# Kernel tuning notes

Hardware: AMD Instinct MI355X
Metric: run time of the kernel (lower is better)

The kernel has to match this reference:

```python
import jax, jax.numpy as jnp
import numpy as np

H, HD, C = 16, 64, 64            # num_heads, head_dim, mini_batch_size
BASE_LR = 1.0
EPS = 1e-6                        # ttt LN eps (ln_fwd / ln_fused_l2_bwd)


def _l2norm(x):
    return x / jnp.maximum(jnp.linalg.norm(x, axis=-1, keepdims=True), 1e-12)


def _ln_fwd(x, g, b):
    mu = x.mean(-1, keepdims=True)
    var = x.var(-1, keepdims=True)
    return g * ((x - mu) * jax.lax.rsqrt(var + EPS)) + b


def _ln_l2_bwd(x, tgt, g, b):
    # gradient of ||LN(x)*g+b - tgt||^2 / 2 wrt x
    D = x.shape[-1]
    mu = x.mean(-1, keepdims=True)
    var = x.var(-1, keepdims=True)
    std = jnp.sqrt(var + EPS)
    xh = (x - mu) / std
    gout = (g * xh + b) - tgt
    gxh = gout * g
    return (D * gxh - gxh.sum(-1, keepdims=True) - xh * (gxh * xh).sum(-1, keepdims=True)) / (D * std)


def setup_inputs() -> dict:
    key = jax.random.key(0)
    ks = jax.random.split(key, 12)
    B, L, D = 4, 8192, 1024
    std = 0.02
    return {
        'hidden_states': jax.random.normal(ks[0], (B, L, D), jnp.float32),
        'wq_w': jax.random.normal(ks[1], (D, D), jnp.float32) * std,
        'wq_b': jnp.zeros((D,), jnp.float32),
        'wk_w': jax.random.normal(ks[2], (D, D), jnp.float32) * std,
        'wk_b': jnp.zeros((D,), jnp.float32),
        'wv_w': jax.random.normal(ks[3], (D, D), jnp.float32) * std,
        'wv_b': jnp.zeros((D,), jnp.float32),
        'wo_w': jax.random.normal(ks[4], (D, D), jnp.float32) * std,
        'wo_b': jnp.zeros((D,), jnp.float32),
        'ttt_norm_weight': jnp.ones((H, HD), jnp.float32),
        'ttt_norm_bias': jnp.zeros((H, HD), jnp.float32),
        'ttt_lr_weight': jax.random.normal(ks[5], (H, 1, D), jnp.float32) * std,
        'ttt_lr_bias': jnp.zeros((H, 1), jnp.float32),
        'W1': jax.random.normal(ks[6], (H, HD, HD), jnp.float32) * std,
        'b1': jnp.zeros((H, 1, HD), jnp.float32),
        'post_norm_w': jnp.ones((D,), jnp.float32),
        'post_norm_b': jnp.zeros((D,), jnp.float32),
    }


def _forward(hidden_states, wq_w, wq_b, wk_w, wk_b, wv_w, wv_b, wo_w, wo_b,
             ttt_norm_weight, ttt_norm_bias, ttt_lr_weight, ttt_lr_bias,
             W1, b1, post_norm_w, post_norm_b):
    B, L, D = hidden_states.shape
    NC = L // C
    XQ = (hidden_states @ wq_w.T + wq_b).reshape(B, L, H, HD)
    XK = (hidden_states @ wk_w.T + wk_b).reshape(B, L, H, HD)
    XV = (hidden_states @ wv_w.T + wv_b).reshape(B, L, H, HD)
    XQ = _l2norm(XQ)
    XK = _l2norm(XK)
    # ln_reconstruction_target (uses sample std, ddof=1, eps=1e-5 on std)
    d = XV - XK
    mu = d.mean(-1, keepdims=True)
    sd = d.std(-1, keepdims=True, ddof=1)
    XV = ttt_norm_weight[None, None] * ((d - mu) / (sd + 1e-5)) + ttt_norm_bias[None, None] + XK
    # reshape to mini-batches: [B,H,NC,C,HD]
    Xmb = hidden_states.reshape(B, NC, C, D)
    to_mb = lambda t: t.transpose(0, 2, 1, 3).reshape(B, H, NC, C, HD)
    XQ, XK, XV = to_mb(XQ), to_mb(XK), to_mb(XV)
    # eta: sigmoid lr gate per token, row-broadcast over mini-batch
    ttt_lr = jax.nn.sigmoid(jnp.einsum('bnkc,hdc->bhnkd', Xmb, ttt_lr_weight)
                            + ttt_lr_bias.reshape(1, H, 1, 1, 1))     # [B,H,NC,C,1]
    eta = jnp.swapaxes(ttt_lr, -1, -2) * (BASE_LR / HD / C)           # [B,H,NC,1,C]
    mask = jnp.tril(jnp.ones((C, C), hidden_states.dtype))
    g = ttt_norm_weight[None, :, None, :]
    bta = ttt_norm_bias[None, :, None, :]
    W0 = jnp.broadcast_to(W1[None], (B, H, HD, HD))
    b0 = jnp.broadcast_to(b1[None], (B, H, 1, HD))

    def step(carry, xs):
        W, bvec = carry
        xq, xk, xv, eta_row = xs                      # eta_row: [B,H,1,C]
        Z1 = xk @ W + bvec                            # [B,H,C,HD]
        grad = _ln_l2_bwd(Z1, xv - xk, g, bta)        # [B,H,C,HD]
        Attn = mask * jnp.einsum('bhid,bhjd->bhij', xq, xk)   # [B,H,C,C]
        eta_full = jnp.broadcast_to(eta_row, Attn.shape)      # [B,H,C,C]
        b1_bar = bvec - (mask * eta_full) @ grad              # [B,H,C,HD]
        Z1_bar = xq @ W - (eta_full * Attn) @ grad + b1_bar
        last_eta = eta_full[..., -1, :, None]                 # [B,H,C,1]
        W_new = W - jnp.einsum('bhcd,bhce->bhde', last_eta * xk, grad)
        b_new = bvec - (last_eta * grad).sum(-2, keepdims=True)
        out = xq + _ln_fwd(Z1_bar, g, bta)
        return (W_new, b_new), out

    xs = (jnp.moveaxis(XQ, 2, 0), jnp.moveaxis(XK, 2, 0),
          jnp.moveaxis(XV, 2, 0), jnp.moveaxis(eta, 2, 0))
    _, outs = jax.lax.scan(step, (W0, b0), xs)        # outs: [NC,B,H,C,HD]
    y = jnp.moveaxis(outs, 0, 2).reshape(B, H, L, HD).transpose(0, 2, 1, 3).reshape(B, L, D)
    # post LayerNorm (eps=1e-6) + output projection
    mu2 = y.mean(-1, keepdims=True)
    var2 = y.var(-1, keepdims=True)
    y = post_norm_w * ((y - mu2) * jax.lax.rsqrt(var2 + 1e-6)) + post_norm_b
    return y @ wo_w.T + wo_b


def reference(hidden_states, wq_w, wq_b, wk_w, wk_b, wv_w, wv_b, wo_w, wo_b,
              ttt_norm_weight, ttt_norm_bias, ttt_lr_weight, ttt_lr_bias,
              W1, b1, post_norm_w, post_norm_b):
    return _forward(hidden_states, wq_w, wq_b, wk_w, wk_b, wv_w, wv_b, wo_w, wo_b,
                    ttt_norm_weight, ttt_norm_bias, ttt_lr_weight, ttt_lr_bias,
                    W1, b1, post_norm_w, post_norm_b)
```

## Files before the change

### kernel.cpp

```cpp
#include <hip/hip_runtime.h>


typedef __attribute__((ext_vector_type(8))) short short8;
typedef __attribute__((ext_vector_type(4))) float f32x4;
typedef __attribute__((ext_vector_type(4))) unsigned short us4;

__device__ __forceinline__ float bf2f(unsigned short s) {
  union { unsigned int u; float f; } c;
  c.u = ((unsigned int)s) << 16;
  return c.f;
}
__device__ __forceinline__ unsigned short f2bf(float f) {
  union { float f; unsigned int u; } c;
  c.f = f;
  unsigned int u = c.u;
  return (unsigned short)((u + 0x7FFFu + ((u >> 16) & 1u)) >> 16);
}

__device__ __forceinline__ void gload_lds16(const void* g, void* l) {
  __builtin_amdgcn_global_load_lds(
      (const __attribute__((address_space(1))) unsigned int*)g,
      (__attribute__((address_space(3))) unsigned int*)l, 16, 0, 0);
}

__device__ __forceinline__ float dpp16_sum(float x) {
  int v = __float_as_int(x);
  x += __int_as_float(__builtin_amdgcn_update_dpp(v, v, 0xB1, 0xF, 0xF, true));
  v = __float_as_int(x);
  x += __int_as_float(__builtin_amdgcn_update_dpp(v, v, 0x4E, 0xF, 0xF, true));
  v = __float_as_int(x);
  x += __int_as_float(__builtin_amdgcn_update_dpp(v, v, 0x141, 0xF, 0xF, true));
  v = __float_as_int(x);
  x += __int_as_float(__builtin_amdgcn_update_dpp(v, v, 0x140, 0xF, 0xF, true));
  return x;
}

__device__ __forceinline__ void barrier_fast() {
  __builtin_amdgcn_sched_barrier(0);
  asm volatile("s_waitcnt lgkmcnt(0)" ::: "memory");
  __builtin_amdgcn_s_barrier();
  asm volatile("" ::: "memory");
  __builtin_amdgcn_sched_barrier(0);
}
__device__ __forceinline__ void bar_nowait() {
  __builtin_amdgcn_sched_barrier(0);
  asm volatile("" ::: "memory");
  __builtin_amdgcn_s_barrier();
  asm volatile("" ::: "memory");
  __builtin_amdgcn_sched_barrier(0);
}

__global__ __launch_bounds__(256) void cvt_f32_bf16(
    const float* __restrict__ in, unsigned short* __restrict__ out, long n) {
  long i = ((long)blockIdx.x * 256 + threadIdx.x) * 4;
  if (i + 3 < n) {
    float4 v = *(const float4*)&in[i];
    us4 o = { f2bf(v.x), f2bf(v.y), f2bf(v.z), f2bf(v.w) };
    *(us4*)&out[i] = o;
  }
}

__global__ __launch_bounds__(256) void build_wcat(
    const float* __restrict__ wq, const float* __restrict__ wk,
    const float* __restrict__ wv, const float* __restrict__ lrw,
    const float* __restrict__ wqb, const float* __restrict__ wkb,
    const float* __restrict__ wvb, const float* __restrict__ lrb,
    unsigned short* __restrict__ Wcat, float* __restrict__ biasc) {
  int i = blockIdx.x * 256 + threadIdx.x;
  int row = i >> 10, col = i & 1023;
  int h = row >> 8, o = row & 255;
  float v;
  if (o < 64)        v = wq[(h * 64 + o) * 1024 + col];
  else if (o < 128)  v = wk[(h * 64 + o - 64) * 1024 + col];
  else if (o < 192)  v = wv[(h * 64 + o - 128) * 1024 + col];
  else if (o == 192) v = lrw[h * 1024 + col];
  else               v = 0.f;
  Wcat[i] = f2bf(v);
  if (i < 4096) {
    int hh = i >> 8, oo = i & 255;
    float bv;
    if (oo < 64)        bv = wqb[hh * 64 + oo];
    else if (oo < 128)  bv = wkb[hh * 64 + oo - 64];
    else if (oo < 192)  bv = wvb[hh * 64 + oo - 128];
    else if (oo == 192) bv = lrb[hh];
    else                bv = 0.f;
    biasc[i] = bv;
  }
}

__global__ __launch_bounds__(512, 1) void gemm256_qkv(
    const unsigned short* __restrict__ A, const unsigned short* __restrict__ B,
    const float* __restrict__ bias, const float* __restrict__ tnw,
    const float* __restrict__ tnb, unsigned short* __restrict__ XQn,
    unsigned short* __restrict__ XKn, unsigned short* __restrict__ TGT,
    float* __restrict__ eta, long M, long K) {
  __shared__ __align__(16) unsigned short g_lds[65536];
  char* ldsc = (char*)g_lds;
  const int tid = threadIdx.x, lane = tid & 63, wid = tid >> 6;
  const int wm = wid >> 2, wn = wid & 3;
  const int l15 = lane & 15, lg = lane >> 4;
  const int NTILN = 16;

  unsigned nwg = gridDim.x, bid = blockIdx.x;
  unsigned cpx = nwg >> 3;
  unsigned swz = (bid & 7) * cpx + (bid >> 3);
  unsigned nidx = swz % (unsigned)NTILN, midx = swz / (unsigned)NTILN;
  const long m0 = (long)midx * 256, n0 = (long)nidx * 256;
  const long ldab = K * 2;

  const int srow = wid * 16 + (lane >> 2);
  const int scol = ((lane & 3) * 16) ^ (((lane >> 3) & 3) << 4);
  const int sdst = wid * 1024;
  const char* Ab = (const char*)A;
  const char* Bb = (const char*)B;

  const int acol = (lg * 16) ^ (((l15 >> 1) & 3) << 4);
  const int aro = (wm * 128 + l15) * 64 + acol;
  const int bro = 65536 + (wn * 64 + l15) * 64 + acol;

#define STG_A(tt, h, bb)                                                      \
  gload_lds16(Ab + (size_t)(m0 + (h) * 128 + srow) * ldab + (size_t)(tt) * 64 \
                  + scol,                                                     \
              ldsc + (bb) * 16384 + (h) * 8192 + sdst)
#define STG_B(tt, h, bb)                                                      \
  gload_lds16(Bb + (size_t)(n0 + (h) * 128 + srow) * ldab + (size_t)(tt) * 64 \
                  + scol,                                                     \
              ldsc + 65536 + (bb) * 16384 + (h) * 8192 + sdst)

  f32x4 acc[8][4];
#pragma unroll
  for (int m = 0; m < 8; ++m)
#pragma unroll
    for (int n = 0; n < 4; ++n) acc[m][n] = (f32x4){0.f, 0.f, 0.f, 0.f};

  const int NT = (int)(K >> 5);

#pragma unroll
  for (int tt = 0; tt < 3; ++tt) {
    STG_A(tt, 0, tt); STG_A(tt, 1, tt);
    STG_B(tt, 0, tt); STG_B(tt, 1, tt);
  }
  asm volatile("s_waitcnt vmcnt(8)" ::: "memory");
  bar_nowait();

#pragma unroll 1
  for (int t = 0; t < NT; ++t) {
    const int buf = t & 3, sb = (t + 3) & 3;
    const bool doStage = (t + 3 < NT);
    const char* ab = ldsc + buf * 16384 + aro;
    const char* bb = ldsc + buf * 16384 + bro;

    short8 av[4], bv[4];
#pragma unroll
    for (int i = 0; i < 4; ++i) av[i] = *(const short8*)(ab + i * 1024);
#pragma unroll
    for (int nf = 0; nf < 4; ++nf) bv[nf] = *(const short8*)(bb + nf * 1024);
    if (doStage) { STG_A(t + 3, 0, sb); STG_A(t + 3, 1, sb); }
    bar_nowait();
    __builtin_amdgcn_s_setprio(1);
#pragma unroll
    for (int i = 0; i < 4; ++i)
#pragma unroll
      for (int nf = 0; nf < 4; ++nf)
        acc[i][nf] = __builtin_amdgcn_mfma_f32_16x16x32_bf16(av[i], bv[nf],
                                                             acc[i][nf], 0, 0, 0);
    __builtin_amdgcn_s_setprio(0);
    bar_nowait();

#pragma unroll
    for (int i = 0; i < 4; ++i) av[i] = *(const short8*)(ab + 4096 + i * 1024);
    if (doStage) { STG_B(t + 3, 0, sb); STG_B(t + 3, 1, sb); }
    bar_nowait();
    __builtin_amdgcn_s_setprio(1);
#pragma unroll
    for (int i = 0; i < 4; ++i)
#pragma unroll
      for (int nf = 0; nf < 4; ++nf)
        acc[4 + i][nf] = __builtin_amdgcn_mfma_f32_16x16x32_bf16(
            av[i], bv[nf], acc[4 + i][nf], 0, 0, 0);
    __builtin_amdgcn_s_setprio(0);
    asm volatile("s_waitcnt vmcnt(8)" ::: "memory");
    bar_nowait();
  }
#undef STG_A
#undef STG_B

  const int h = (int)nidx;
  float bcol[4], twv[4], tbv[4];
#pragma unroll
  for (int nf = 0; nf < 4; ++nf) {
    bcol[nf] = bias[n0 + wn * 64 + nf * 16 + l15];
    twv[nf] = tnw[h * 64 + nf * 16 + l15];
    tbv[nf] = tnb[h * 64 + nf * 16 + l15];
  }
  __syncthreads();
  unsigned short* kn_s = g_lds;

  if (wn == 0) {
#pragma unroll
    for (int mf = 0; mf < 8; ++mf)
#pragma unroll
      for (int j = 0; j < 4; ++j) {
        float v[4], s2 = 0.f;
#pragma unroll
        for (int nf = 0; nf < 4; ++nf) {
          v[nf] = acc[mf][nf][j] + bcol[nf];
          s2 += v[nf] * v[nf];
        }
        s2 = dpp16_sum(s2);
        float rn = 1.f / fmaxf(sqrtf(s2), 1e-12f);
        size_t tt = (size_t)(m0 + wm * 128 + mf * 16 + lg * 4 + j);
#pragma unroll
        for (int nf = 0; nf < 4; ++nf)
          XQn[tt * 1024 + h * 64 + nf * 16 + l15] = f2bf(v[nf] * rn);
      }
  } else if (wn == 1) {
#pragma unroll
    for (int mf = 0; mf < 8; ++mf)
#pragma unroll
      for (int j = 0; j < 4; ++j) {
        float v[4], s2 = 0.f;
#pragma unroll
        for (int nf = 0; nf < 4; ++nf) {
          v[nf] = acc[mf][nf][j] + bcol[nf];
          s2 += v[nf] * v[nf];
        }
        s2 = dpp16_sum(s2);
        float rn = 1.f / fmaxf(sqrtf(s2), 1e-12f);
        size_t tt = (size_t)(m0 + wm * 128 + mf * 16 + lg * 4 + j);
        int lr_ = wm * 128 + mf * 16 + lg * 4 + j;
#pragma unroll
        for (int nf = 0; nf < 4; ++nf) {
          unsigned short kb = f2bf(v[nf] * rn);
          XKn[tt * 1024 + h * 64 + nf * 16 + l15] = kb;
          kn_s[lr_ * 72 + nf * 16 + l15] = kb;
        }
      }
  }
  __syncthreads();
  if (wn == 2) {
#pragma unroll
    for (int mf = 0; mf < 8; ++mf)
#pragma unroll
      for (int j = 0; j < 4; ++j) {
        int lr_ = wm * 128 + mf * 16 + lg * 4 + j;
        float dv[4], s1 = 0.f, s2 = 0.f;
#pragma unroll
        for (int nf = 0; nf < 4; ++nf) {
          float kn = bf2f(kn_s[lr_ * 72 + nf * 16 + l15]);
          dv[nf] = acc[mf][nf][j] + bcol[nf] - kn;
          s1 += dv[nf];
          s2 += dv[nf] * dv[nf];
        }
        s1 = dpp16_sum(s1);
        s2 = dpp16_sum(s2);
        float mu = s1 * 0.015625f;
        float var1 = fmaxf(s2 - 64.f * mu * mu, 0.f) * (1.f / 63.f);
        float rs = 1.f / (sqrtf(var1) + 1e-5f);
        size_t tt = (size_t)(m0 + wm * 128 + mf * 16 + lg * 4 + j);
#pragma unroll
        for (int nf = 0; nf < 4; ++nf)
          TGT[tt * 1024 + h * 64 + nf * 16 + l15] =
              f2bf(twv[nf] * ((dv[nf] - mu) * rs) + tbv[nf]);
      }
  } else if (wn == 3 && l15 == 0) {
#pragma unroll
    for (int mf = 0; mf < 8; ++mf)
#pragma unroll
      for (int j = 0; j < 4; ++j) {
        size_t tt = (size_t)(m0 + wm * 128 + mf * 16 + lg * 4 + j);
        float lgt = acc[mf][0][j] + bcol[0];
        float sig = 1.f / (1.f + expf(-lgt));
        eta[((tt >> 13) * 16 + h) * 8192 + (tt & 8191)] = sig * (1.f / 4096.f);
      }
  }
}

template <int WRITE_BF16>
__global__ __launch_bounds__(512, 1) void gemm256(
    const unsigned short* __restrict__ A, const unsigned short* __restrict__ B,
    const float* __restrict__ bias, void* __restrict__ Cout,
    long M, long N, long K, int NTILN, long ldc) {
  __shared__ __align__(16) unsigned short g_lds[65536];
  char* ldsc = (char*)g_lds;
  const int tid = threadIdx.x, lane = tid & 63, wid = tid >> 6;
  const int wm = wid >> 2, wn = wid & 3;
  const int l15 = lane & 15, lg = lane >> 4;

  unsigned nwg = gridDim.x, bid = blockIdx.x;
  unsigned cpx = nwg >> 3;
  unsigned swz = (bid & 7) * cpx + (bid >> 3);
  unsigned nidx = swz % (unsigned)NTILN, midx = swz / (unsigned)NTILN;
  const long m0 = (long)midx * 256, n0 = (long)nidx * 256;
  const long ldab = K * 2;

  const int srow = wid * 16 + (lane >> 2);
  const int scol = ((lane & 3) * 16) ^ (((lane >> 3) & 3) << 4);
  const int sdst = wid * 1024;
  const char* Ab = (const char*)A;
  const char* Bb = (const char*)B;

  const int acol = (lg * 16) ^ (((l15 >> 1) & 3) << 4);
  const int aro = (wm * 128 + l15) * 64 + acol;
  const int bro = 65536 + (wn * 64 + l15) * 64 + acol;

#define STG_A(tt, h, bb)                                                      \
  gload_lds16(Ab + (size_t)(m0 + (h) * 128 + srow) * ldab + (size_t)(tt) * 64 \
                  + scol,                                                     \
              ldsc + (bb) * 16384 + (h) * 8192 + sdst)
#define STG_B(tt, h, bb)                                                      \
  gload_lds16(Bb + (size_t)(n0 + (h) * 128 + srow) * ldab + (size_t)(tt) * 64 \
                  + scol,                                                     \
              ldsc + 65536 + (bb) * 16384 + (h) * 8192 + sdst)

  f32x4 acc[8][4];
#pragma unroll
  for (int m = 0; m < 8; ++m)
#pragma unroll
    for (int n = 0; n < 4; ++n) acc[m][n] = (f32x4){0.f, 0.f, 0.f, 0.f};

  const int NT = (int)(K >> 5);

#pragma unroll
  for (int tt = 0; tt < 3; ++tt) {
    STG_A(tt, 0, tt); STG_A(tt, 1, tt);
    STG_B(tt, 0, tt); STG_B(tt, 1, tt);
  }
  asm volatile("s_waitcnt vmcnt(8)" ::: "memory");
  bar_nowait();

#pragma unroll 1
  for (int t = 0; t < NT; ++t) {
    const int buf = t & 3, sb = (t + 3) & 3;
    const bool doStage = (t + 3 < NT);
    const char* ab = ldsc + buf * 16384 + aro;
    const char* bb = ldsc + buf * 16384 + bro;

    short8 av[4], bv[4];
#pragma unroll
    for (int i = 0; i < 4; ++i) av[i] = *(const short8*)(ab + i * 1024);
#pragma unroll
    for (int nf = 0; nf < 4; ++nf) bv[nf] = *(const short8*)(bb + nf * 1024);
    if (doStage) { STG_A(t + 3, 0, sb); STG_A(t + 3, 1, sb); }
    bar_nowait();
    __builtin_amdgcn_s_setprio(1);
#pragma unroll
    for (int i = 0; i < 4; ++i)
#pragma unroll
      for (int nf = 0; nf < 4; ++nf)
        acc[i][nf] = __builtin_amdgcn_mfma_f32_16x16x32_bf16(av[i], bv[nf],
                                                             acc[i][nf], 0, 0, 0);
    __builtin_amdgcn_s_setprio(0);
    bar_nowait();

#pragma unroll
    for (int i = 0; i < 4; ++i) av[i] = *(const short8*)(ab + 4096 + i * 1024);
    if (doStage) { STG_B(t + 3, 0, sb); STG_B(t + 3, 1, sb); }
    bar_nowait();
    __builtin_amdgcn_s_setprio(1);
#pragma unroll
    for (int i = 0; i < 4; ++i)
#pragma unroll
      for (int nf = 0; nf < 4; ++nf)
        acc[4 + i][nf] = __builtin_amdgcn_mfma_f32_16x16x32_bf16(
            av[i], bv[nf], acc[4 + i][nf], 0, 0, 0);
    __builtin_amdgcn_s_setprio(0);
    asm volatile("s_waitcnt vmcnt(8)" ::: "memory");
    bar_nowait();
  }
#undef STG_A
#undef STG_B

#pragma unroll
  for (int mf = 0; mf < 8; ++mf) {
    long r0 = m0 + wm * 128 + mf * 16 + lg * 4;
#pragma unroll
    for (int nf = 0; nf < 4; ++nf) {
      long c = n0 + wn * 64 + nf * 16 + l15;
      float bvv = bias ? bias[c] : 0.f;
#pragma unroll
      for (int j = 0; j < 4; ++j) {
        float v = acc[mf][nf][j] + bvv;
        if (WRITE_BF16)
          ((unsigned short*)Cout)[(r0 + j) * ldc + c] = f2bf(v);
        else
          ((float*)Cout)[(r0 + j) * ldc + c] = v;
      }
    }
  }
}

__global__ __launch_bounds__(512, 1) void ttt_scan(
    const unsigned short* __restrict__ XQ, const unsigned short* __restrict__ XK,
    const unsigned short* __restrict__ TG, const float* __restrict__ eta_buf,
    const float* __restrict__ W1, const float* __restrict__ b1,
    const float* __restrict__ tnw, const float* __restrict__ tnb,
    float* __restrict__ y) {
  const int bh = blockIdx.x;
  const int b = bh >> 4, h = bh & 15;
  const int tid = threadIdx.x;
  const int lane = tid & 63, wid = tid >> 6;
  const bool isA = wid < 4;
  const int q = wid & 3;
  const int l15 = lane & 15, lg = lane >> 4;

  __shared__ __align__(16) unsigned short xq_s[2][64 * 72];
  __shared__ __align__(16) unsigned short tg_s[2][64 * 72];
  __shared__ __align__(16) unsigned short xk_s[2][64 * 72];
  __shared__ __align__(16) unsigned short gc_s[64 * 72];
  __shared__ __align__(16) unsigned short gradT[64 * 72];
  __shared__ __align__(16) unsigned short xkTe[64 * 72];
  __shared__ __align__(16) unsigned short WT_b[2][64 * 72];
  __shared__ float eta_s[2][64];
  __shared__ float bpart[4][64];

  const size_t tokb = (size_t)b * 8192;
  const int col0 = h * 64;
  const int rr_ = q * 16 + (lane >> 3);
  const int c8_ = (lane & 7) * 8;

  short8 pA0[2], pA1[2], pB0[2];
  float peta = 0.f;
  float bstv[4], gwv[4], gbv[4];
  f32x4 Wreg[4];

  if (isA) {
#pragma unroll
    for (int n = 0; n < 4; ++n) {
      int e = n * 16 + l15;
      bstv[n] = b1[h * 64 + e];
      gwv[n] = tnw[h * 64 + e];
      gbv[n] = tnb[h * 64 + e];
    }
#pragma unroll
    for (int j = 0; j < 2; ++j) {
      size_t g = (tokb + rr_ + j * 8) * 1024 + col0 + c8_;
      pA0[j] = *(const short8*)&XQ[g];
      pA1[j] = *(const short8*)&TG[g];
    }
#pragma unroll
    for (int j = 0; j < 2; ++j) {
      int rr = rr_ + j * 8;
      *(short8*)&xq_s[0][rr * 72 + c8_] = pA0[j];
      *(short8*)&tg_s[0][rr * 72 + c8_] = pA1[j];
    }
#pragma unroll
    for (int j = 0; j < 2; ++j) {
      size_t g = (tokb + 64 + rr_ + j * 8) * 1024 + col0 + c8_;
      pA0[j] = *(const short8*)&XQ[g];
      pA1[j] = *(const short8*)&TG[g];
    }
  } else {
#pragma unroll
    for (int j = 0; j < 2; ++j)
      pB0[j] = *(const short8*)&XK[(tokb + rr_ + j * 8) * 1024 + col0 + c8_];
#pragma unroll
    for (int j = 0; j < 2; ++j)
      *(short8*)&xk_s[0][(rr_ + j * 8) * 72 + c8_] = pB0[j];
#pragma unroll
    for (int j = 0; j < 2; ++j)
      pB0[j] = *(const short8*)&XK[(tokb + 64 + rr_ + j * 8) * 1024 + col0 + c8_];
#pragma unroll
    for (int n = 0; n < 4; ++n)
#pragma unroll
      for (int jj = 0; jj < 4; ++jj) {
        int d = q * 16 + lg * 4 + jj, e = n * 16 + l15;
        float w = W1[h * 4096 + d * 64 + e];
        Wreg[n][jj] = w;
        WT_b[0][e * 72 + d] = f2bf(w);
      }
    if (wid == 4) {
      eta_s[0][lane] = eta_buf[(size_t)bh * 8192 + lane];
      peta = eta_buf[(size_t)bh * 8192 + 64 + lane];
    }
  }
  __syncthreads();

  for (int nc = 0; nc < 128; ++nc) {
    const int p = nc & 1;
    const unsigned short* WTc = WT_b[p];
    unsigned short* WTn = WT_b[p ^ 1];

    if (isA) {
      if (nc) {
#pragma unroll
        for (int n = 0; n < 4; ++n) {
          int e = n * 16 + l15;
          bstv[n] -= bpart[0][e] + bpart[1][e] + bpart[2][e] + bpart[3][e];
        }
      }
      if (nc + 1 < 128) {
#pragma unroll
        for (int j = 0; j < 2; ++j) {
          int rr = rr_ + j * 8;
          *(short8*)&xq_s[p ^ 1][rr * 72 + c8_] = pA0[j];
          *(short8*)&tg_s[p ^ 1][rr * 72 + c8_] = pA1[j];
        }
      }
      if (nc + 2 < 128) {
#pragma unroll
        for (int j = 0; j < 2; ++j) {
          size_t g = (tokb + (nc + 2) * 64 + rr_ + j * 8) * 1024 + col0 + c8_;
          pA0[j] = *(const short8*)&XQ[g];
          pA1[j] = *(const short8*)&TG[g];
        }
      }
      f32x4 accZ[4];
#pragma unroll
      for (int n = 0; n < 4; ++n)
        accZ[n] = (f32x4){bstv[n], bstv[n], bstv[n], bstv[n]};
      __builtin_amdgcn_s_setprio(1);
#pragma unroll
      for (int kk = 0; kk < 2; ++kk) {
        const int ko = kk * 32 + lg * 8;
        short8 a_xk = *(const short8*)&xk_s[p][(q * 16 + l15) * 72 + ko];
#pragma unroll
        for (int n = 0; n < 4; ++n) {
          short8 b_w = *(const short8*)&WTc[(n * 16 + l15) * 72 + ko];
          accZ[n] = __builtin_amdgcn_mfma_f32_16x16x32_bf16(a_xk, b_w, accZ[n], 0, 0, 0);
        }
      }
      __builtin_amdgcn_s_setprio(0);
      float grv[4][4];
#pragma unroll
      for (int j = 0; j < 4; ++j) {
        const int r = q * 16 + lg * 4 + j;
        float z[4], s1 = 0.f, s2 = 0.f;
#pragma unroll
        for (int n = 0; n < 4; ++n) {
          z[n] = accZ[n][j];
          s1 += z[n];
          s2 += z[n] * z[n];
        }
        s1 = dpp16_sum(s1);
        s2 = dpp16_sum(s2);
        float mu = s1 * 0.015625f;
        float var = s2 * 0.015625f - mu * mu;
        float rstd = rsqrtf(var + 1e-6f);
        float xh[4], gx[4], s3 = 0.f, s4 = 0.f;
#pragma unroll
        for (int n = 0; n < 4; ++n) {
          xh[n] = (z[n] - mu) * rstd;
          float tg = bf2f(tg_s[p][r * 72 + n * 16 + l15]);
          float go = gwv[n] * xh[n] + gbv[n] - tg;
          gx[n] = go * gwv[n];
          s3 += gx[n];
          s4 += gx[n] * xh[n];
        }
        s3 = dpp16_sum(s3);
        s4 = dpp16_sum(s4);
#pragma unroll
        for (int n = 0; n < 4; ++n)
          grv[n][j] = (64.f * gx[n] - s3 - xh[n] * s4) * rstd * 0.015625f;
      }
#pragma unroll
      for (int n = 0; n < 4; ++n) {
        us4 pk = {f2bf(grv[n][0]), f2bf(grv[n][1]), f2bf(grv[n][2]),
                  f2bf(grv[n][3])};
        *(us4*)&gradT[(n * 16 + l15) * 72 + q * 16 + lg * 4] = pk;
      }
    } else {
      if (nc + 1 < 128) {
#pragma unroll
        for (int j = 0; j < 2; ++j)
          *(short8*)&xk_s[p ^ 1][(rr_ + j * 8) * 72 + c8_] = pB0[j];
        if (wid == 4) eta_s[p ^ 1][lane] = peta;
      }
      if (nc + 2 < 128) {
#pragma unroll
        for (int j = 0; j < 2; ++j)
          pB0[j] = *(const short8*)
              &XK[(tokb + (nc + 2) * 64 + rr_ + j * 8) * 1024 + col0 + c8_];
        if (wid == 4) peta = eta_buf[(size_t)bh * 8192 + (nc + 2) * 64 + lane];
      }
#pragma unroll
      for (int it = 0; it < 4; ++it) {
        int c0 = q * 16 + it * 4;
        us4 pk;
#pragma unroll
        for (int u = 0; u < 4; ++u)
          pk[u] = f2bf(-eta_s[p][c0 + u] * bf2f(xk_s[p][(c0 + u) * 72 + lane]));
        *(us4*)&xkTe[lane * 72 + c0] = pk;
      }
      f32x4 accA[4];
#pragma unroll
      for (int n = 0; n < 4; ++n) accA[n] = (f32x4){0.f, 0.f, 0.f, 0.f};
      __builtin_amdgcn_s_setprio(1);
#pragma unroll
      for (int kk = 0; kk < 2; ++kk) {
        const int ko = kk * 32 + lg * 8;
        short8 a_xq = *(const short8*)&xq_s[p][(q * 16 + l15) * 72 + ko];
#pragma unroll
        for (int n = 0; n < 4; ++n) {
          short8 b_k = *(const short8*)&xk_s[p][(n * 16 + l15) * 72 + ko];
          accA[n] = __builtin_amdgcn_mfma_f32_16x16x32_bf16(a_xq, b_k, accA[n], 0, 0, 0);
        }
      }
      __builtin_amdgcn_s_setprio(0);
#pragma unroll
      for (int j = 0; j < 4; ++j) {
        const int r = q * 16 + lg * 4 + j;
#pragma unroll
        for (int n = 0; n < 4; ++n) {
          int cj = n * 16 + l15;
          float v = (cj <= r) ? (-eta_s[p][cj] * (1.f + accA[n][j])) : 0.f;
          gc_s[r * 72 + cj] = f2bf(v);
        }
      }
    }
    barrier_fast();

    if (isA) {
      f32x4 accZb[4];
#pragma unroll
      for (int n = 0; n < 4; ++n)
        accZb[n] = (f32x4){bstv[n], bstv[n], bstv[n], bstv[n]};
      __builtin_amdgcn_s_setprio(1);
#pragma unroll
      for (int kk = 0; kk < 2; ++kk) {
        const int ko = kk * 32 + lg * 8;
        short8 a_xq = *(const short8*)&xq_s[p][(q * 16 + l15) * 72 + ko];
        short8 a_gc = *(const short8*)&gc_s[(q * 16 + l15) * 72 + ko];
#pragma unroll
        for (int n = 0; n < 4; ++n) {
          short8 b_w = *(const short8*)&WTc[(n * 16 + l15) * 72 + ko];
          short8 b_g = *(const short8*)&gradT[(n * 16 + l15) * 72 + ko];
          accZb[n] = __builtin_amdgcn_mfma_f32_16x16x32_bf16(a_xq, b_w, accZb[n], 0, 0, 0);
          accZb[n] = __builtin_amdgcn_mfma_f32_16x16x32_bf16(a_gc, b_g, accZb[n], 0, 0, 0);
        }
      }
      __builtin_amdgcn_s_setprio(0);
#pragma unroll
      for (int j = 0; j < 4; ++j) {
        const int r = q * 16 + lg * 4 + j;
        float z[4], s1 = 0.f, s2 = 0.f;
#pragma unroll
        for (int n = 0; n < 4; ++n) {
          z[n] = accZb[n][j];
          s1 += z[n];
          s2 += z[n] * z[n];
        }
        s1 = dpp16_sum(s1);
        s2 = dpp16_sum(s2);
        float mu = s1 * 0.015625f;
        float var = s2 * 0.015625f - mu * mu;
        float rstd = rsqrtf(var + 1e-6f);
        size_t gbase = (tokb + nc * 64 + r) * 1024 + col0;
#pragma unroll
        for (int n = 0; n < 4; ++n) {
          int e = n * 16 + l15;
          float ov = bf2f(xq_s[p][r * 72 + e]) + gwv[n] * ((z[n] - mu) * rstd) + gbv[n];
          y[gbase + e] = ov;
        }
      }
    } else {
      short8 a_ke[2], b_g[2][4];
#pragma unroll
      for (int kk = 0; kk < 2; ++kk) {
        const int ko = kk * 32 + lg * 8;
        a_ke[kk] = *(const short8*)&xkTe[(q * 16 + l15) * 72 + ko];
#pragma unroll
        for (int n = 0; n < 4; ++n)
          b_g[kk][n] = *(const short8*)&gradT[(n * 16 + l15) * 72 + ko];
      }
      f32x4 accW[4];
#pragma unroll
      for (int n = 0; n < 4; ++n) accW[n] = Wreg[n];
      __builtin_amdgcn_s_setprio(1);
#pragma unroll
      for (int kk = 0; kk < 2; ++kk)
#pragma unroll
        for (int n = 0; n < 4; ++n)
          accW[n] = __builtin_amdgcn_mfma_f32_16x16x32_bf16(a_ke[kk], b_g[kk][n],
                                                            accW[n], 0, 0, 0);
      __builtin_amdgcn_s_setprio(0);
#pragma unroll
      for (int n = 0; n < 4; ++n) {
        Wreg[n] = accW[n];
        us4 pk = {f2bf(accW[n][0]), f2bf(accW[n][1]), f2bf(accW[n][2]),
                  f2bf(accW[n][3])};
        *(us4*)&WTn[(n * 16 + l15) * 72 + q * 16 + lg * 4] = pk;
      }
      {
        float s = 0.f;
#pragma unroll
        for (int it = 0; it < 4; ++it) {
          us4 gv = *(const us4*)&gradT[lane * 72 + q * 16 + it * 4];
#pragma unroll
          for (int u = 0; u < 4; ++u)
            s += eta_s[p][q * 16 + it * 4 + u] * bf2f(gv[u]);
        }
        bpart[q][lane] = s;
      }
    }
    barrier_fast();
  }
}

__global__ __launch_bounds__(256) void postnorm(
    const float* __restrict__ yv, const float* __restrict__ pw,
    const float* __restrict__ pb, unsigned short* __restrict__ yn) {
  int t = blockIdx.x;
  int tid = threadIdx.x, lane = tid & 63, wid = tid >> 6;
  const float* row = yv + (size_t)t * 1024;
  float4 v = *(const float4*)&row[tid * 4];
  float s1 = v.x + v.y + v.z + v.w;
  float s2 = v.x * v.x + v.y * v.y + v.z * v.z + v.w * v.w;
#pragma unroll
  for (int o = 1; o < 64; o <<= 1) {
    s1 += __shfl_xor(s1, o);
    s2 += __shfl_xor(s2, o);
  }
  __shared__ float r1[4], r2[4];
  if (lane == 0) {
    r1[wid] = s1;
    r2[wid] = s2;
  }
  __syncthreads();
  s1 = r1[0] + r1[1] + r1[2] + r1[3];
  s2 = r2[0] + r2[1] + r2[2] + r2[3];
  float mu = s1 * (1.f / 1024.f);
  float var = s2 * (1.f / 1024.f) - mu * mu;
  float rstd = rsqrtf(var + 1e-6f);
  int c = tid * 4;
  us4 o4 = {f2bf(pw[c] * ((v.x - mu) * rstd) + pb[c]),
            f2bf(pw[c + 1] * ((v.y - mu) * rstd) + pb[c + 1]),
            f2bf(pw[c + 2] * ((v.z - mu) * rstd) + pb[c + 2]),
            f2bf(pw[c + 3] * ((v.w - mu) * rstd) + pb[c + 3])};
  *(us4*)&yn[(size_t)t * 1024 + c] = o4;
}

extern "C" void kernel_launch(void* const* d_in, const int* in_sizes, int n_in,
                              void* d_out, int out_size, void* d_ws,
                              size_t ws_size, hipStream_t stream) {
  const float* hs  = (const float*)d_in[0];
  const float* wqw = (const float*)d_in[1];
  const float* wqb = (const float*)d_in[2];
  const float* wkw = (const float*)d_in[3];
  const float* wkb = (const float*)d_in[4];
  const float* wvw = (const float*)d_in[5];
  const float* wvb = (const float*)d_in[6];
  const float* wow = (const float*)d_in[7];
  const float* wob = (const float*)d_in[8];
  const float* tnw = (const float*)d_in[9];
  const float* tnb = (const float*)d_in[10];
  const float* lrw = (const float*)d_in[11];
  const float* lrb = (const float*)d_in[12];
  const float* W1  = (const float*)d_in[13];
  const float* b1  = (const float*)d_in[14];
  const float* pnw = (const float*)d_in[15];
  const float* pnb = (const float*)d_in[16];

  const size_t OFF_XQ    = 0;
  const size_t OFF_XK    = 67108864;
  const size_t OFF_TGT   = 134217728;
  const size_t OFF_ETA   = 201326592;
  const size_t OFF_WOBF  = OFF_ETA + 2097152;
  const size_t OFF_HSBF  = OFF_WOBF + 2097152;
  const size_t OFF_WCAT  = OFF_HSBF + 67108864;
  const size_t OFF_BIASC = OFF_WCAT + 8388608;
  const size_t OFF_YV    = OFF_HSBF;
  const size_t NEEDED_A  = OFF_BIASC + 16384;
  const size_t NEEDED_B  = OFF_YV + 134217728;
  const size_t NEEDED    = NEEDED_A > NEEDED_B ? NEEDED_A : NEEDED_B;
  if (ws_size < NEEDED) return;

  char* ws = (char*)d_ws;
  unsigned short* XQn   = (unsigned short*)(ws + OFF_XQ);
  unsigned short* ynorm = (unsigned short*)(ws + OFF_XQ);
  unsigned short* XKn   = (unsigned short*)(ws + OFF_XK);
  unsigned short* TGT   = (unsigned short*)(ws + OFF_TGT);
  float* eta_buf        = (float*)(ws + OFF_ETA);
  unsigned short* wo_bf = (unsigned short*)(ws + OFF_WOBF);
  unsigned short* hs_bf = (unsigned short*)(ws + OFF_HSBF);
  unsigned short* Wcat  = (unsigned short*)(ws + OFF_WCAT);
  float* biasc          = (float*)(ws + OFF_BIASC);
  float* yv             = (float*)(ws + OFF_YV);

  cvt_f32_bf16<<<32768, 256, 0, stream>>>(hs, hs_bf, 33554432L);
  build_wcat<<<16384, 256, 0, stream>>>(wqw, wkw, wvw, lrw, wqb, wkb, wvb, lrb,
                                        Wcat, biasc);
  cvt_f32_bf16<<<1024, 256, 0, stream>>>(wow, wo_bf, 1048576L);
  gemm256_qkv<<<2048, 512, 0, stream>>>(hs_bf, Wcat, biasc, tnw, tnb,
                                        XQn, XKn, TGT, eta_buf, 32768L, 1024L);
  ttt_scan<<<64, 512, 0, stream>>>(XQn, XKn, TGT, eta_buf, W1, b1, tnw, tnb, yv);
  postnorm<<<32768, 256, 0, stream>>>(yv, pnw, pnb, ynorm);
  gemm256<0><<<512, 512, 0, stream>>>(ynorm, wo_bf, wob, d_out,
                                      32768L, 1024L, 1024L, 4, 1024L);
}
```

Baseline: 889.4 us.

## Stage projection epilogue through LDS for coalesced stores and swizzle xkTe

The QKV projection epilogue now writes normalized Q, K and the LN target into LDS tiles, then copies them to global memory as 16-byte row-contiguous chunks. This replaces scattered 2-byte stores, and idle waves handle the Q/K copy while the target is computed. Separately, the transposed eta*xk tile in the scan kernel gets an XOR swizzle on its 4-element groups to reduce LDS bank conflicts on the write and the MFMA operand read. The cost is an extra barrier, more LDS traffic, and a chance that the swizzle indexing is wrong.

```diff
diff --git a/kernel.cpp b/kernel.cpp
--- a/kernel.cpp
+++ b/kernel.cpp
@@ -194,7 +194,9 @@
     tbv[nf] = tnb[h * 64 + nf * 16 + l15];
   }
   __syncthreads();
-  unsigned short* kn_s = g_lds;
+  unsigned short* kn_t = g_lds;
+  unsigned short* qn_t = g_lds + 18432;
+  unsigned short* tg_t = g_lds + 36864;
 
   if (wn == 0) {
 #pragma unroll
@@ -209,10 +211,10 @@
         }
         s2 = dpp16_sum(s2);
         float rn = 1.f / fmaxf(sqrtf(s2), 1e-12f);
-        size_t tt = (size_t)(m0 + wm * 128 + mf * 16 + lg * 4 + j);
+        int lr_ = wm * 128 + mf * 16 + lg * 4 + j;
 #pragma unroll
         for (int nf = 0; nf < 4; ++nf)
-          XQn[tt * 1024 + h * 64 + nf * 16 + l15] = f2bf(v[nf] * rn);
+          qn_t[lr_ * 72 + nf * 16 + l15] = f2bf(v[nf] * rn);
       }
   } else if (wn == 1) {
 #pragma unroll
@@ -227,17 +229,24 @@
         }
         s2 = dpp16_sum(s2);
         float rn = 1.f / fmaxf(sqrtf(s2), 1e-12f);
+        int lr_ = wm * 128 + mf * 16 + lg * 4 + j;
+#pragma unroll
+        for (int nf = 0; nf < 4; ++nf)
+          kn_t[lr_ * 72 + nf * 16 + l15] = f2bf(v[nf] * rn);
+      }
+  } else if (wn == 3 && l15 == 0) {
+#pragma unroll
+    for (int mf = 0; mf < 8; ++mf)
+#pragma unroll
+      for (int j = 0; j < 4; ++j) {
         size_t tt = (size_t)(m0 + wm * 128 + mf * 16 + lg * 4 + j);
-        int lr_ = wm * 128 + mf * 16 + lg * 4 + j;
-#pragma unroll
-        for (int nf = 0; nf < 4; ++nf) {
-          unsigned short kb = f2bf(v[nf] * rn);
-          XKn[tt * 1024 + h * 64 + nf * 16 + l15] = kb;
-          kn_s[lr_ * 72 + nf * 16 + l15] = kb;
-        }
+        float lgt = acc[mf][0][j] + bcol[0];
+        float sig = 1.f / (1.f + expf(-lgt));
+        eta[((tt >> 13) * 16 + h) * 8192 + (tt & 8191)] = sig * (1.f / 4096.f);
       }
   }
   __syncthreads();
+
   if (wn == 2) {
 #pragma unroll
     for (int mf = 0; mf < 8; ++mf)
@@ -247,7 +256,7 @@
         float dv[4], s1 = 0.f, s2 = 0.f;
 #pragma unroll
         for (int nf = 0; nf < 4; ++nf) {
-          float kn = bf2f(kn_s[lr_ * 72 + nf * 16 + l15]);
+          float kn = bf2f(kn_t[lr_ * 72 + nf * 16 + l15]);
           dv[nf] = acc[mf][nf][j] + bcol[nf] - kn;
           s1 += dv[nf];
           s2 += dv[nf] * dv[nf];
@@ -257,22 +266,27 @@
         float mu = s1 * 0.015625f;
         float var1 = fmaxf(s2 - 64.f * mu * mu, 0.f) * (1.f / 63.f);
         float rs = 1.f / (sqrtf(var1) + 1e-5f);
-        size_t tt = (size_t)(m0 + wm * 128 + mf * 16 + lg * 4 + j);
 #pragma unroll
         for (int nf = 0; nf < 4; ++nf)
-          TGT[tt * 1024 + h * 64 + nf * 16 + l15] =
+          tg_t[lr_ * 72 + nf * 16 + l15] =
               f2bf(twv[nf] * ((dv[nf] - mu) * rs) + tbv[nf]);
       }
-  } else if (wn == 3 && l15 == 0) {
-#pragma unroll
-    for (int mf = 0; mf < 8; ++mf)
-#pragma unroll
-      for (int j = 0; j < 4; ++j) {
-        size_t tt = (size_t)(m0 + wm * 128 + mf * 16 + lg * 4 + j);
-        float lgt = acc[mf][0][j] + bcol[0];
-        float sig = 1.f / (1.f + expf(-lgt));
-        eta[((tt >> 13) * 16 + h) * 8192 + (tt & 8191)] = sig * (1.f / 4096.f);
-      }
+  } else {
+    int wlin = wid - (wid >= 3) - (wid >= 7);
+    const unsigned short* src = (wlin < 3) ? qn_t : kn_t;
+    unsigned short* dst = (wlin < 3) ? XQn : XKn;
+    int wl = wlin % 3;
+    for (int c = wl * 64 + lane; c < 2048; c += 192) {
+      int r = c >> 3, ch = c & 7;
+      short8 v = *(const short8*)&src[r * 72 + ch * 8];
+      *(short8*)&dst[(m0 + r) * 1024 + h * 64 + ch * 8] = v;
+    }
+  }
+  __syncthreads();
+  for (int c = tid; c < 2048; c += 512) {
+    int r = c >> 3, ch = c & 7;
+    short8 v = *(const short8*)&tg_t[r * 72 + ch * 8];
+    *(short8*)&TGT[(m0 + r) * 1024 + h * 64 + ch * 8] = v;
   }
 }
 
@@ -573,14 +587,17 @@
               &XK[(tokb + (nc + 2) * 64 + rr_ + j * 8) * 1024 + col0 + c8_];
         if (wid == 4) peta = eta_buf[(size_t)bh * 8192 + (nc + 2) * 64 + lane];
       }
-#pragma unroll
-      for (int it = 0; it < 4; ++it) {
-        int c0 = q * 16 + it * 4;
-        us4 pk;
-#pragma unroll
-        for (int u = 0; u < 4; ++u)
-          pk[u] = f2bf(-eta_s[p][c0 + u] * bf2f(xk_s[p][(c0 + u) * 72 + lane]));
-        *(us4*)&xkTe[lane * 72 + c0] = pk;
+      {
+        const int sxk = ((lane >> 3) & 3) << 1;
+#pragma unroll
+        for (int it = 0; it < 4; ++it) {
+          int c0 = q * 16 + it * 4;
+          us4 pk;
+#pragma unroll
+          for (int u = 0; u < 4; ++u)
+            pk[u] = f2bf(-eta_s[p][c0 + u] * bf2f(xk_s[p][(c0 + u) * 72 + lane]));
+          *(us4*)&xkTe[lane * 72 + (((q * 4 + it) ^ sxk) << 2)] = pk;
+        }
       }
       f32x4 accA[4];
 #pragma unroll
@@ -654,14 +671,15 @@
         }
       }
     } else {
+      const int scons = ((2 * q + (l15 >> 3)) & 3) << 1;
       short8 a_ke[2], b_g[2][4];
 #pragma unroll
       for (int kk = 0; kk < 2; ++kk) {
-        const int ko = kk * 32 + lg * 8;
-        a_ke[kk] = *(const short8*)&xkTe[(q * 16 + l15) * 72 + ko];
+        const int gb = (kk * 8 + lg * 2) ^ scons;
+        a_ke[kk] = *(const short8*)&xkTe[(q * 16 + l15) * 72 + (gb << 2)];
 #pragma unroll
         for (int n = 0; n < 4; ++n)
-          b_g[kk][n] = *(const short8*)&gradT[(n * 16 + l15) * 72 + ko];
+          b_g[kk][n] = *(const short8*)&gradT[(n * 16 + l15) * 72 + kk * 32 + lg * 8];
       }
       f32x4 accW[4];
 #pragma unroll
```

New measurement: 901.3 us. About the same (+1.3%).

## Switch GEMM mainloops to 3-stage interleaved A/B LDS pipeline with one barrier

Applied to the files above, without the earlier changes.

Both 256x256 GEMM kernels move from a 4-deep buffer ring with A and B in separate LDS regions to a 3-deep ring where each stage holds A and B together. Each iteration now issues all four stage loads up front, reads all eight A fragments at once, runs 32 MFMAs in one block and hits a single barrier instead of three. The LDS footprint shrinks from 128 KB to 96 KB. The trade-offs are a shallower prefetch distance, more live A registers, and a possible read-after-overwrite race, since stage t+2 is issued into a buffer without a fresh barrier.

```diff
diff --git a/kernel.cpp b/kernel.cpp
--- a/kernel.cpp
+++ b/kernel.cpp
@@ -88,13 +88,14 @@
   }
 }
 
+
 __global__ __launch_bounds__(512, 1) void gemm256_qkv(
     const unsigned short* __restrict__ A, const unsigned short* __restrict__ B,
     const float* __restrict__ bias, const float* __restrict__ tnw,
     const float* __restrict__ tnb, unsigned short* __restrict__ XQn,
     unsigned short* __restrict__ XKn, unsigned short* __restrict__ TGT,
     float* __restrict__ eta, long M, long K) {
-  __shared__ __align__(16) unsigned short g_lds[65536];
+  __shared__ __align__(16) unsigned short g_lds[49152];
   char* ldsc = (char*)g_lds;
   const int tid = threadIdx.x, lane = tid & 63, wid = tid >> 6;
   const int wm = wid >> 2, wn = wid & 3;
@@ -116,16 +117,16 @@
 
   const int acol = (lg * 16) ^ (((l15 >> 1) & 3) << 4);
   const int aro = (wm * 128 + l15) * 64 + acol;
-  const int bro = 65536 + (wn * 64 + l15) * 64 + acol;
+  const int bro = 16384 + (wn * 64 + l15) * 64 + acol;
 
 #define STG_A(tt, h, bb)                                                      \
   gload_lds16(Ab + (size_t)(m0 + (h) * 128 + srow) * ldab + (size_t)(tt) * 64 \
                   + scol,                                                     \
-              ldsc + (bb) * 16384 + (h) * 8192 + sdst)
+              ldsc + (bb) * 32768 + (h) * 8192 + sdst)
 #define STG_B(tt, h, bb)                                                      \
   gload_lds16(Bb + (size_t)(n0 + (h) * 128 + srow) * ldab + (size_t)(tt) * 64 \
                   + scol,                                                     \
-              ldsc + 65536 + (bb) * 16384 + (h) * 8192 + sdst)
+              ldsc + (bb) * 32768 + 16384 + (h) * 8192 + sdst)
 
   f32x4 acc[8][4];
 #pragma unroll
@@ -135,52 +136,37 @@
 
   const int NT = (int)(K >> 5);
 
-#pragma unroll
-  for (int tt = 0; tt < 3; ++tt) {
-    STG_A(tt, 0, tt); STG_A(tt, 1, tt);
-    STG_B(tt, 0, tt); STG_B(tt, 1, tt);
-  }
-  asm volatile("s_waitcnt vmcnt(8)" ::: "memory");
+  STG_A(0, 0, 0); STG_A(0, 1, 0); STG_B(0, 0, 0); STG_B(0, 1, 0);
+  STG_A(1, 0, 1); STG_A(1, 1, 1); STG_B(1, 0, 1); STG_B(1, 1, 1);
+  asm volatile("s_waitcnt vmcnt(4)" ::: "memory");
   bar_nowait();
 
+  int buf = 0, sb = 2;
 #pragma unroll 1
   for (int t = 0; t < NT; ++t) {
-    const int buf = t & 3, sb = (t + 3) & 3;
-    const bool doStage = (t + 3 < NT);
-    const char* ab = ldsc + buf * 16384 + aro;
-    const char* bb = ldsc + buf * 16384 + bro;
-
-    short8 av[4], bv[4];
-#pragma unroll
-    for (int i = 0; i < 4; ++i) av[i] = *(const short8*)(ab + i * 1024);
-#pragma unroll
-    for (int nf = 0; nf < 4; ++nf) bv[nf] = *(const short8*)(bb + nf * 1024);
-    if (doStage) { STG_A(t + 3, 0, sb); STG_A(t + 3, 1, sb); }
-    bar_nowait();
+    if (t + 2 < NT) {
+      STG_A(t + 2, 0, sb); STG_A(t + 2, 1, sb);
+      STG_B(t + 2, 0, sb); STG_B(t + 2, 1, sb);
+    }
+    const char* ab = ldsc + buf * 32768 + aro;
+    const char* bb2 = ldsc + buf * 32768 + bro;
+    short8 av[8], bv[4];
+#pragma unroll
+    for (int i = 0; i < 8; ++i) av[i] = *(const short8*)(ab + i * 1024);
+#pragma unroll
+    for (int nf = 0; nf < 4; ++nf) bv[nf] = *(const short8*)(bb2 + nf * 1024);
     __builtin_amdgcn_s_setprio(1);
 #pragma unroll
-    for (int i = 0; i < 4; ++i)
+    for (int i = 0; i < 8; ++i)
 #pragma unroll
       for (int nf = 0; nf < 4; ++nf)
         acc[i][nf] = __builtin_amdgcn_mfma_f32_16x16x32_bf16(av[i], bv[nf],
                                                              acc[i][nf], 0, 0, 0);
     __builtin_amdgcn_s_setprio(0);
+    asm volatile("s_waitcnt vmcnt(4)" ::: "memory");
     bar_nowait();
-
-#pragma unroll
-    for (int i = 0; i < 4; ++i) av[i] = *(const short8*)(ab + 4096 + i * 1024);
-    if (doStage) { STG_B(t + 3, 0, sb); STG_B(t + 3, 1, sb); }
-    bar_nowait();
-    __builtin_amdgcn_s_setprio(1);
-#pragma unroll
-    for (int i = 0; i < 4; ++i)
-#pragma unroll
-      for (int nf = 0; nf < 4; ++nf)
-        acc[4 + i][nf] = __builtin_amdgcn_mfma_f32_16x16x32_bf16(
-            av[i], bv[nf], acc[4 + i][nf], 0, 0, 0);
-    __builtin_amdgcn_s_setprio(0);
-    asm volatile("s_waitcnt vmcnt(8)" ::: "memory");
-    bar_nowait();
+    buf = (buf == 2) ? 0 : buf + 1;
+    sb = (sb == 2) ? 0 : sb + 1;
   }
 #undef STG_A
 #undef STG_B
@@ -281,7 +267,7 @@
     const unsigned short* __restrict__ A, const unsigned short* __restrict__ B,
     const float* __restrict__ bias, void* __restrict__ Cout,
     long M, long N, long K, int NTILN, long ldc) {
-  __shared__ __align__(16) unsigned short g_lds[65536];
+  __shared__ __align__(16) unsigned short g_lds[49152];
   char* ldsc = (char*)g_lds;
   const int tid = threadIdx.x, lane = tid & 63, wid = tid >> 6;
   const int wm = wid >> 2, wn = wid & 3;
@@ -302,16 +288,16 @@
 
   const int acol = (lg * 16) ^ (((l15 >> 1) & 3) << 4);
   const int aro = (wm * 128 + l15) * 64 + acol;
-  const int bro = 65536 + (wn * 64 + l15) * 64 + acol;
+  const int bro = 16384 + (wn * 64 + l15) * 64 + acol;
 
 #define STG_A(tt, h, bb)                                                      \
   gload_lds16(Ab + (size_t)(m0 + (h) * 128 + srow) * ldab + (size_t)(tt) * 64 \
                   + scol,                                                     \
-              ldsc + (bb) * 16384 + (h) * 8192 + sdst)
+              ldsc + (bb) * 32768 + (h) * 8192 + sdst)
 #define STG_B(tt, h, bb)                                                      \
   gload_lds16(Bb + (size_t)(n0 + (h) * 128 + srow) * ldab + (size_t)(tt) * 64 \
                   + scol,                                                     \
-              ldsc + 65536 + (bb) * 16384 + (h) * 8192 + sdst)
+              ldsc + (bb) * 32768 + 16384 + (h) * 8192 + sdst)
 
   f32x4 acc[8][4];
 #pragma unroll
@@ -321,52 +307,37 @@
 
   const int NT = (int)(K >> 5);
 
-#pragma unroll
-  for (int tt = 0; tt < 3; ++tt) {
-    STG_A(tt, 0, tt); STG_A(tt, 1, tt);
-    STG_B(tt, 0, tt); STG_B(tt, 1, tt);
-  }
-  asm volatile("s_waitcnt vmcnt(8)" ::: "memory");
+  STG_A(0, 0, 0); STG_A(0, 1, 0); STG_B(0, 0, 0); STG_B(0, 1, 0);
+  STG_A(1, 0, 1); STG_A(1, 1, 1); STG_B(1, 0, 1); STG_B(1, 1, 1);
+  asm volatile("s_waitcnt vmcnt(4)" ::: "memory");
   bar_nowait();
 
+  int buf = 0, sb = 2;
 #pragma unroll 1
   for (int t = 0; t < NT; ++t) {
-    const int buf = t & 3, sb = (t + 3) & 3;
-    const bool doStage = (t + 3 < NT);
-    const char* ab = ldsc + buf * 16384 + aro;
-    const char* bb = ldsc + buf * 16384 + bro;
-
-    short8 av[4], bv[4];
-#pragma unroll
-    for (int i = 0; i < 4; ++i) av[i] = *(const short8*)(ab + i * 1024);
-#pragma unroll
-    for (int nf = 0; nf < 4; ++nf) bv[nf] = *(const short8*)(bb + nf * 1024);
-    if (doStage) { STG_A(t + 3, 0, sb); STG_A(t + 3, 1, sb); }
-    bar_nowait();
+    if (t + 2 < NT) {
+      STG_A(t + 2, 0, sb); STG_A(t + 2, 1, sb);
+      STG_B(t + 2, 0, sb); STG_B(t + 2, 1, sb);
+    }
+    const char* ab = ldsc + buf * 32768 + aro;
+    const char* bb2 = ldsc + buf * 32768 + bro;
+    short8 av[8], bv[4];
+#pragma unroll
+    for (int i = 0; i < 8; ++i) av[i] = *(const short8*)(ab + i * 1024);
+#pragma unroll
+    for (int nf = 0; nf < 4; ++nf) bv[nf] = *(const short8*)(bb2 + nf * 1024);
     __builtin_amdgcn_s_setprio(1);
 #pragma unroll
-    for (int i = 0; i < 4; ++i)
+    for (int i = 0; i < 8; ++i)
 #pragma unroll
       for (int nf = 0; nf < 4; ++nf)
         acc[i][nf] = __builtin_amdgcn_mfma_f32_16x16x32_bf16(av[i], bv[nf],
                                                              acc[i][nf], 0, 0, 0);
     __builtin_amdgcn_s_setprio(0);
+    asm volatile("s_waitcnt vmcnt(4)" ::: "memory");
     bar_nowait();
-
-#pragma unroll
-    for (int i = 0; i < 4; ++i) av[i] = *(const short8*)(ab + 4096 + i * 1024);
-    if (doStage) { STG_B(t + 3, 0, sb); STG_B(t + 3, 1, sb); }
-    bar_nowait();
-    __builtin_amdgcn_s_setprio(1);
-#pragma unroll
-    for (int i = 0; i < 4; ++i)
-#pragma unroll
-      for (int nf = 0; nf < 4; ++nf)
-        acc[4 + i][nf] = __builtin_amdgcn_mfma_f32_16x16x32_bf16(
-            av[i], bv[nf], acc[4 + i][nf], 0, 0, 0);
-    __builtin_amdgcn_s_setprio(0);
-    asm volatile("s_waitcnt vmcnt(8)" ::: "memory");
-    bar_nowait();
+    buf = (buf == 2) ? 0 : buf + 1;
+    sb = (sb == 2) ? 0 : sb + 1;
   }
 #undef STG_A
 #undef STG_B
```

New measurement: 889.1 us. About the same (-0.0%).
